# Performance work log

Hardware: AMD Instinct MI355X
Metric: run time of the kernel (lower is better)

Reference implementation:

```python
import jax, jax.numpy as jnp
import numpy as np

DIM = 192
HEADS = 6
WS = 7        # window_size
SS = 3        # shift_size
MLP_RATIO = 4.0
B = 64
H_RES = 56
W_RES = 56
EPS = 1e-5


def _rel_index(ws):
    # standard Swin relative position index, (ws*ws, ws*ws) int
    coords = np.stack(np.meshgrid(np.arange(ws), np.arange(ws), indexing='ij'))  # 2,ws,ws
    flat = coords.reshape(2, -1)                                                 # 2,N
    rel = (flat[:, :, None] - flat[:, None, :]).transpose(1, 2, 0)               # N,N,2
    rel[:, :, 0] += ws - 1
    rel[:, :, 1] += ws - 1
    rel[:, :, 0] *= 2 * ws - 1
    return rel.sum(-1)  # N,N


def _attn_mask(H, W, ws, ss):
    # (num_windows, N, N) float mask with 0 / -100, static given H,W,ws,ss
    img = np.zeros((H, W))
    sl = (slice(0, -ws), slice(-ws, -ss), slice(-ss, None))
    cnt = 0
    for hs in sl:
        for wsl in sl:
            img[hs, wsl] = cnt
            cnt += 1
    mw = img.reshape(H // ws, ws, W // ws, ws).transpose(0, 2, 1, 3).reshape(-1, ws * ws)
    diff = mw[:, None, :] - mw[:, :, None]
    return jnp.asarray(np.where(diff != 0, -100.0, 0.0).astype(np.float32))


def _ln(x, g, b):
    mu = x.mean(-1, keepdims=True)
    var = jnp.var(x, axis=-1, keepdims=True)
    return (x - mu) * jax.lax.rsqrt(var + EPS) * g + b


def setup_inputs() -> dict:
    key = jax.random.key(0)
    ks = jax.random.split(key, 8)
    C = DIM
    hid = int(C * MLP_RATIO)
    nrm = lambda k, s: jax.random.normal(k, s, jnp.float32) * 0.02
    return {
        "x": jax.random.normal(ks[0], (B, H_RES * W_RES, C), jnp.float32),
        "norm1_g": jnp.ones((C,), jnp.float32),
        "norm1_b": jnp.zeros((C,), jnp.float32),
        "qkv_w": nrm(ks[1], (3 * C, C)),
        "qkv_b": jnp.zeros((3 * C,), jnp.float32),
        "rel_bias_table": nrm(ks[2], ((2 * WS - 1) ** 2, HEADS)),
        "proj_w": nrm(ks[3], (C, C)),
        "proj_b": jnp.zeros((C,), jnp.float32),
        "norm2_g": jnp.ones((C,), jnp.float32),
        "norm2_b": jnp.zeros((C,), jnp.float32),
        "fc1_w": nrm(ks[4], (hid, C)),
        "fc1_b": jnp.zeros((hid,), jnp.float32),
        "fc2_w": nrm(ks[5], (C, hid)),
        "fc2_b": jnp.zeros((C,), jnp.float32),
        "H": H_RES,
        "W": W_RES,
    }


def _block(x, norm1_g, norm1_b, qkv_w, qkv_b, rel_bias_table, proj_w, proj_b,
           norm2_g, norm2_b, fc1_w, fc1_b, fc2_w, fc2_b, H, W):
    Bn, L, C = x.shape
    ws = min(WS, H, W)
    ss = SS if ws > SS else 0
    nH, nW = H // ws, W // ws
    N = ws * ws
    hd = C // HEADS

    shortcut = x
    h = _ln(x, norm1_g, norm1_b).reshape(Bn, H, W, C)
    if ss > 0:
        h = jnp.roll(h, (-ss, -ss), axis=(1, 2))
    # window partition -> (Bn*nH*nW, N, C)
    win = h.reshape(Bn, nH, ws, nW, ws, C).transpose(0, 1, 3, 2, 4, 5).reshape(-1, N, C)

    qkv = win @ qkv_w.T + qkv_b                       # (nWin, N, 3C)
    qkv = qkv.reshape(-1, N, 3, HEADS, hd).transpose(2, 0, 3, 1, 4)
    q, k, v = qkv[0], qkv[1], qkv[2]                  # (nWin, heads, N, hd)
    scale = float(hd) ** -0.5
    attn = jnp.einsum('whnd,whmd->whnm', q * scale, k)

    idx = _rel_index(ws)                              # N,N (static)
    bias = rel_bias_table[idx.reshape(-1)].reshape(N, N, HEADS).transpose(2, 0, 1)
    attn = attn + bias[None]

    if ss > 0:
        mask = _attn_mask(H, W, ws, ss)               # (nH*nW, N, N)
        attn = attn.reshape(Bn, nH * nW, HEADS, N, N) + mask[None, :, None]
        attn = attn.reshape(-1, HEADS, N, N)

    attn = jax.nn.softmax(attn, axis=-1)
    out = jnp.einsum('whnm,whmd->whnd', attn, v)      # (nWin, heads, N, hd)
    out = out.transpose(0, 2, 1, 3).reshape(-1, N, C)
    out = out @ proj_w.T + proj_b

    # window reverse -> (Bn, H, W, C)
    out = out.reshape(Bn, nH, nW, ws, ws, C).transpose(0, 1, 3, 2, 4, 5).reshape(Bn, H, W, C)
    if ss > 0:
        out = jnp.roll(out, (ss, ss), axis=(1, 2))
    x = shortcut + out.reshape(Bn, H * W, C)

    h2 = _ln(x, norm2_g, norm2_b)
    h2 = jax.nn.gelu(h2 @ fc1_w.T + fc1_b, approximate=False)
    h2 = h2 @ fc2_w.T + fc2_b
    return x + h2


def reference(x, norm1_g, norm1_b, qkv_w, qkv_b, rel_bias_table, proj_w, proj_b,
              norm2_g, norm2_b, fc1_w, fc1_b, fc2_w, fc2_b, H, W):
    return _block(x, norm1_g, norm1_b, qkv_w, qkv_b, rel_bias_table, proj_w, proj_b,
                  norm2_g, norm2_b, fc1_w, fc1_b, fc2_w, fc2_b, H, W)
```

## Files before the change

### kernel.cpp

```cpp
#include <hip/hip_runtime.h>
#include <hip/hip_bf16.h>
#include <math.h>

typedef __attribute__((ext_vector_type(8))) short short8;
typedef __attribute__((ext_vector_type(4))) float floatx4;

__device__ __forceinline__ float bf2f(unsigned short u) {
    union { unsigned int i; float f; } v;
    v.i = ((unsigned int)u) << 16;
    return v.f;
}
__device__ __forceinline__ unsigned short f2bf(float f) {
    union { float f; unsigned int i; } v;
    v.f = f;
    return (unsigned short)((v.i + 0x7FFFu + ((v.i >> 16) & 1u)) >> 16);
}
__device__ __forceinline__ void async16(const void* g, void* l) {
    __builtin_amdgcn_global_load_lds((const __attribute__((address_space(1))) void*)g,
                                     (__attribute__((address_space(3))) void*)l, 16, 0, 0);
}

__global__ __launch_bounds__(256) void cvt_kernel(const float* __restrict__ s,
                                                  unsigned short* __restrict__ d, int n,
                                                  int cut, float scale) {
    int i = blockIdx.x * 256 + threadIdx.x;
    if (i < n) d[i] = f2bf(s[i] * (i < cut ? scale : 1.0f));
}
__global__ __launch_bounds__(256) void biasscale_kernel(const float* __restrict__ s,
                                                        float* __restrict__ d, int n,
                                                        int cut, float scale) {
    int i = blockIdx.x * 256 + threadIdx.x;
    if (i < n) d[i] = s[i] * (i < cut ? scale : 1.0f);
}

__global__ __launch_bounds__(256) void bmt_kernel(const float* __restrict__ btab,
                                                  float* __restrict__ tbl) {
    int idx = blockIdx.x * 256 + threadIdx.x;
    int key = idx & 63;
    int q = (idx >> 6) & 63;
    int h = (idx >> 12) % 6;
    int cls = idx / (4096 * 6);
    float v;
    if (key >= 49) v = -3.0e38f;
    else if (q >= 49) v = 0.0f;
    else {
        int qi = q / 7, qj = q % 7, ki = key / 7, kj = key % 7;
        v = btab[((qi - ki + 6) * 13 + (qj - kj + 6)) * 6 + h];
        int whT = (cls >> 1) & 1, wwT = cls & 1;
        int rq = (whT ? (qi < 4 ? 1 : 2) : 0) * 3 + (wwT ? (qj < 4 ? 1 : 2) : 0);
        int rk = (whT ? (ki < 4 ? 1 : 2) : 0) * 3 + (wwT ? (kj < 4 ? 1 : 2) : 0);
        if (rq != rk) v -= 100.0f;
    }
    tbl[idx] = v;
}

__global__ __launch_bounds__(256) void ln_kernel(const float* __restrict__ src,
                                                 const float* __restrict__ gw,
                                                 const float* __restrict__ bw,
                                                 unsigned short* __restrict__ dst,
                                                 int mode) {
    int o = blockIdx.x * 4 + (threadIdx.x >> 6);
    int lane = threadIdx.x & 63;
    size_t srow;
    if (mode == 0) {
        int win = o / 49, n = o % 49;
        int b = win >> 6, wl = win & 63;
        int wh = wl >> 3, ww = wl & 7;
        int i = n / 7, j = n % 7;
        int pr = (wh * 7 + i + 3) % 56;
        int pc = (ww * 7 + j + 3) % 56;
        srow = ((size_t)b * 3136 + (size_t)(pr * 56 + pc)) * 192;
    } else {
        srow = (size_t)o * 192;
    }
    float v0 = src[srow + lane];
    float v1 = src[srow + lane + 64];
    float v2 = src[srow + lane + 128];
    float s = v0 + v1 + v2;
    float s2 = v0 * v0 + v1 * v1 + v2 * v2;
    #pragma unroll
    for (int off = 32; off > 0; off >>= 1) {
        s += __shfl_xor(s, off);
        s2 += __shfl_xor(s2, off);
    }
    float mean = s * (1.0f / 192.0f);
    float var = s2 * (1.0f / 192.0f) - mean * mean;
    float inv = rsqrtf(var + 1e-5f);
    size_t drow = (size_t)o * 192;
    dst[drow + lane]       = f2bf((v0 - mean) * inv * gw[lane]       + bw[lane]);
    dst[drow + lane + 64]  = f2bf((v1 - mean) * inv * gw[lane + 64]  + bw[lane + 64]);
    dst[drow + lane + 128] = f2bf((v2 - mean) * inv * gw[lane + 128] + bw[lane + 128]);
}

template <int EPI>
__global__ __launch_bounds__(256) void gemm_nt(const unsigned short* __restrict__ A,
                                               const unsigned short* __restrict__ W,
                                               const float* __restrict__ bias,
                                               int K, int ldo, int mbase,
                                               unsigned short* __restrict__ outb,
                                               float* __restrict__ outf,
                                               const float* __restrict__ resid) {
    __shared__ __align__(16) unsigned short Al[128][32];
    __shared__ __align__(16) unsigned short Wl[64][32];
    int tid = threadIdx.x;
    int lane = tid & 63;
    int wv = tid >> 6;
    int wm = wv >> 1, wn = wv & 1;
    int m0 = blockIdx.y * 128;
    int n0 = blockIdx.x * 64;
    int quad = lane >> 4, l15 = lane & 15;

    int srow = lane >> 2;
    int scol = (lane & 3) * 8;
    const unsigned short* aP0 = A + (size_t)(m0 + wv * 32 + srow) * K + scol;
    const unsigned short* aP1 = aP0 + (size_t)16 * K;
    const unsigned short* wP  = W + (size_t)(n0 + wv * 16 + srow) * K + scol;
    unsigned short* lA0 = &Al[wv * 32][0];
    unsigned short* lA1 = &Al[wv * 32 + 16][0];
    unsigned short* lW  = &Wl[wv * 16][0];

    floatx4 acc[4][2];
    floatx4 zero = {0.f, 0.f, 0.f, 0.f};
    #pragma unroll
    for (int a = 0; a < 4; ++a)
        #pragma unroll
        for (int b = 0; b < 2; ++b) acc[a][b] = zero;

    for (int kt = 0; kt < K; kt += 32) {
        __syncthreads();
        async16(aP0 + kt, lA0);
        async16(aP1 + kt, lA1);
        async16(wP + kt, lW);
        __syncthreads();
        short8 af[4], wf[2];
        #pragma unroll
        for (int mt = 0; mt < 4; ++mt)
            af[mt] = *(const short8*)&Al[wm * 64 + mt * 16 + l15][quad * 8];
        #pragma unroll
        for (int nt = 0; nt < 2; ++nt)
            wf[nt] = *(const short8*)&Wl[wn * 32 + nt * 16 + l15][quad * 8];
        #pragma unroll
        for (int mt = 0; mt < 4; ++mt)
            #pragma unroll
            for (int nt = 0; nt < 2; ++nt)
                acc[mt][nt] = __builtin_amdgcn_mfma_f32_16x16x32_bf16(af[mt], wf[nt], acc[mt][nt], 0, 0, 0);
    }

    #pragma unroll
    for (int mt = 0; mt < 4; ++mt) {
        #pragma unroll
        for (int nt = 0; nt < 2; ++nt) {
            #pragma unroll
            for (int r = 0; r < 4; ++r) {
                int m = m0 + wm * 64 + mt * 16 + quad * 4 + r;
                int n = n0 + wn * 32 + nt * 16 + l15;
                float v = acc[mt][nt][r] + bias[n];
                if (EPI == 0) {
                    outb[(size_t)m * ldo + n] = f2bf(v);
                } else if (EPI == 1) {
                    float g = 0.5f * v * (1.0f + erff(v * 0.70710678118654752f));
                    outb[(size_t)m * ldo + n] = f2bf(g);
                } else if (EPI == 2) {
                    int win = m / 49, np = m % 49;
                    int b = win >> 6, wl = win & 63;
                    int wh = wl >> 3, ww = wl & 7;
                    int i = np / 7, j = np % 7;
                    int pr = (wh * 7 + i + 3) % 56;
                    int pc = (ww * 7 + j + 3) % 56;
                    size_t dst = ((size_t)b * 3136 + (size_t)(pr * 56 + pc)) * 192 + n;
                    outf[dst] = resid[dst] + v;
                } else {
                    size_t dst = (size_t)(mbase + m) * ldo + n;
                    outf[dst] = resid[dst] + v;
                }
            }
        }
    }
}

__global__ __launch_bounds__(192) void attn_kernel(const unsigned short* __restrict__ qkv,
                                                   const float* __restrict__ tbl,
                                                   unsigned short* __restrict__ awin) {
    __shared__ __align__(16) unsigned short Pb[3][64][72];
    int w = blockIdx.x >> 1;
    int hb = (blockIdx.x & 1) * 3;
    int hl = threadIdx.x >> 6;
    int h = hb + hl;
    int lane = threadIdx.x & 63;
    int quad = lane >> 4, l15 = lane & 15;
    const unsigned short* base = qkv + (size_t)w * 49 * 576;
    int wl = w & 63;
    int cls = ((wl >> 3) == 7 ? 2 : 0) + ((wl & 7) == 7 ? 1 : 0);
    const float* tb = tbl + (size_t)(cls * 6 + h) * 4096;

    short8 kf[4], qf[4];
    #pragma unroll
    for (int mt = 0; mt < 4; ++mt)
        kf[mt] = *(const short8*)(base + (size_t)(mt * 16 + l15) * 576 + 192 + h * 32 + quad * 8);
    #pragma unroll
    for (int nt = 0; nt < 4; ++nt)
        qf[nt] = *(const short8*)(base + (size_t)(nt * 16 + l15) * 576 + h * 32 + quad * 8);

    floatx4 S[4][4];
    #pragma unroll
    for (int mt = 0; mt < 4; ++mt)
        #pragma unroll
        for (int nt = 0; nt < 4; ++nt) {
            floatx4 cinit = *(const floatx4*)(tb + (nt * 16 + l15) * 64 + mt * 16 + quad * 4);
            S[mt][nt] = __builtin_amdgcn_mfma_f32_16x16x32_bf16(kf[mt], qf[nt], cinit, 0, 0, 0);
        }

    #pragma unroll
    for (int mt = 0; mt < 4; ++mt)
        #pragma unroll
        for (int nt = 0; nt < 4; ++nt)
            #pragma unroll
            for (int rr = 0; rr < 4; ++rr)
                S[mt][nt][rr] = __expf(S[mt][nt][rr]);

    float rinv[4];
    #pragma unroll
    for (int nt = 0; nt < 4; ++nt) {
        float s = 0.f;
        #pragma unroll
        for (int mt = 0; mt < 4; ++mt)
            s += (S[mt][nt][0] + S[mt][nt][1]) + (S[mt][nt][2] + S[mt][nt][3]);
        s += __shfl_xor(s, 16);
        s += __shfl_xor(s, 32);
        rinv[nt] = 1.0f / s;
    }

    #pragma unroll
    for (int mt = 0; mt < 4; ++mt) {
        #pragma unroll
        for (int nt = 0; nt < 4; ++nt) {
            __hip_bfloat162 p0 = __float22bfloat162_rn(
                make_float2(S[mt][nt][0] * rinv[nt], S[mt][nt][1] * rinv[nt]));
            __hip_bfloat162 p1 = __float22bfloat162_rn(
                make_float2(S[mt][nt][2] * rinv[nt], S[mt][nt][3] * rinv[nt]));
            union { __hip_bfloat162 h2[2]; uint2 u; } pk;
            pk.h2[0] = p0;
            pk.h2[1] = p1;
            *(uint2*)&Pb[hl][nt * 16 + l15][mt * 16 + quad * 4] = pk.u;
        }
    }

    floatx4 O[4][2];
    floatx4 zero = {0.f, 0.f, 0.f, 0.f};
    #pragma unroll
    for (int mt = 0; mt < 4; ++mt)
        #pragma unroll
        for (int nt = 0; nt < 2; ++nt) O[mt][nt] = zero;
    #pragma unroll
    for (int ks = 0; ks < 2; ++ks) {
        short8 vf[2];
        #pragma unroll
        for (int nt = 0; nt < 2; ++nt) {
            const unsigned short* vb =
                base + (size_t)(ks * 32 + quad * 8) * 576 + 384 + h * 32 + nt * 16 + l15;
            #pragma unroll
            for (int j = 0; j < 8; ++j) vf[nt][j] = (short)vb[(size_t)j * 576];
        }
        #pragma unroll
        for (int mt = 0; mt < 4; ++mt) {
            short8 pf = *(const short8*)&Pb[hl][mt * 16 + l15][ks * 32 + quad * 8];
            #pragma unroll
            for (int nt = 0; nt < 2; ++nt)
                O[mt][nt] = __builtin_amdgcn_mfma_f32_16x16x32_bf16(pf, vf[nt], O[mt][nt], 0, 0, 0);
        }
    }
    #pragma unroll
    for (int mt = 0; mt < 4; ++mt) {
        #pragma unroll
        for (int rr = 0; rr < 4; ++rr) {
            int q = mt * 16 + quad * 4 + rr;
            if (q < 49) {
                #pragma unroll
                for (int nt = 0; nt < 2; ++nt)
                    awin[((size_t)w * 49 + q) * 192 + h * 32 + nt * 16 + l15] =
                        f2bf(O[mt][nt][rr]);
            }
        }
    }
}

extern "C" void kernel_launch(void* const* d_in, const int* in_sizes, int n_in,
                              void* d_out, int out_size, void* d_ws, size_t ws_size,
                              hipStream_t stream) {
    const float* x      = (const float*)d_in[0];
    const float* n1g    = (const float*)d_in[1];
    const float* n1b    = (const float*)d_in[2];
    const float* qkv_w  = (const float*)d_in[3];
    const float* qkv_b  = (const float*)d_in[4];
    const float* btab   = (const float*)d_in[5];
    const float* proj_w = (const float*)d_in[6];
    const float* proj_b = (const float*)d_in[7];
    const float* n2g    = (const float*)d_in[8];
    const float* n2b    = (const float*)d_in[9];
    const float* fc1_w  = (const float*)d_in[10];
    const float* fc1_b  = (const float*)d_in[11];
    const float* fc2_w  = (const float*)d_in[12];
    const float* fc2_b  = (const float*)d_in[13];
    float* out = (float*)d_out;

    char* p = (char*)d_ws;
    size_t off = 0;
    auto alloc = [&](size_t bytes) {
        char* r = p + off;
        off = (off + bytes + 255) & ~(size_t)255;
        return r;
    };
    unsigned short* wq   = (unsigned short*)alloc((size_t)576 * 192 * 2);
    unsigned short* wp   = (unsigned short*)alloc((size_t)192 * 192 * 2);
    unsigned short* w1   = (unsigned short*)alloc((size_t)768 * 192 * 2);
    unsigned short* w2   = (unsigned short*)alloc((size_t)192 * 768 * 2);
    unsigned short* hwin = (unsigned short*)alloc((size_t)200704 * 192 * 2);
    unsigned short* qkvb = (unsigned short*)alloc((size_t)200704 * 576 * 2);
    float*          xres = (float*)alloc((size_t)200704 * 192 * 4);
    unsigned short* g1   = (unsigned short*)alloc((size_t)50176 * 768 * 2);
    if (ws_size < off) return;
    float* tbl   = (float*)g1;
    float* qkvbs = (float*)g1 + 98304;

    const float scale = 0.17677669529663687f;
    cvt_kernel<<<432, 256, 0, stream>>>(qkv_w, wq, 110592, 36864, scale);
    cvt_kernel<<<144, 256, 0, stream>>>(proj_w, wp, 36864, 0, 1.0f);
    cvt_kernel<<<576, 256, 0, stream>>>(fc1_w, w1, 147456, 0, 1.0f);
    cvt_kernel<<<576, 256, 0, stream>>>(fc2_w, w2, 147456, 0, 1.0f);
    biasscale_kernel<<<3, 256, 0, stream>>>(qkv_b, qkvbs, 576, 192, scale);
    bmt_kernel<<<384, 256, 0, stream>>>(btab, tbl);

    ln_kernel<<<50176, 256, 0, stream>>>(x, n1g, n1b, hwin, 0);
    gemm_nt<0><<<dim3(9, 1568), 256, 0, stream>>>(hwin, wq, qkvbs, 192, 576, 0, qkvb, nullptr, nullptr);
    attn_kernel<<<8192, 192, 0, stream>>>(qkvb, tbl, hwin );
    gemm_nt<2><<<dim3(3, 1568), 256, 0, stream>>>(hwin, wp, proj_b, 192, 192, 0, nullptr, xres, x);
    unsigned short* h2 = qkvb;
    ln_kernel<<<50176, 256, 0, stream>>>(xres, n2g, n2b, h2, 1);
    for (int c = 0; c < 4; ++c) {
        int mb = c * 50176;
        gemm_nt<1><<<dim3(12, 392), 256, 0, stream>>>(h2 + (size_t)mb * 192, w1, fc1_b, 192, 768, 0,
                                                      g1, nullptr, nullptr);
        gemm_nt<3><<<dim3(3, 392), 256, 0, stream>>>(g1, w2, fc2_b, 768, 192, mb,
                                                     nullptr, out, xres);
    }
}
```

Baseline: 1.103 ms.

## Write V transposed from QKV GEMM and fuse proj GEMM with LayerNorm2

The QKV GEMM epilogue now writes V into a per-window, per-head transposed buffer, so attention loads V fragments with vector reads instead of strided scalar gathers. Q and K rows are clamped rather than read past the window. The projection GEMM is merged with the residual add and the second LayerNorm in one kernel that computes full 192-wide rows, which removes a separate LN pass over xres. h2 is written in image order and the MLP reads it from there. The cost is an extra zeroing kernel for V padding, scattered scalar V stores, and the xres buffer being reused for vT before proj_ln overwrites it.

```diff
diff --git a/kernel.cpp b/kernel.cpp
--- a/kernel.cpp
+++ b/kernel.cpp
@@ -31,6 +31,13 @@
                                                         int cut, float scale) {
     int i = blockIdx.x * 256 + threadIdx.x;
     if (i < n) d[i] = s[i] * (i < cut ? scale : 1.0f);
+}
+
+__global__ __launch_bounds__(256) void zerov_kernel(unsigned short* __restrict__ vT) {
+    int idx = blockIdx.x * 256 + threadIdx.x;
+    size_t row = (size_t)(idx >> 1);
+    uint4 z = make_uint4(0u, 0u, 0u, 0u);
+    *(uint4*)(vT + row * 64 + 48 + (idx & 1) * 8) = z;
 }
 
 __global__ __launch_bounds__(256) void bmt_kernel(const float* __restrict__ btab,
@@ -57,22 +64,16 @@
 __global__ __launch_bounds__(256) void ln_kernel(const float* __restrict__ src,
                                                  const float* __restrict__ gw,
                                                  const float* __restrict__ bw,
-                                                 unsigned short* __restrict__ dst,
-                                                 int mode) {
+                                                 unsigned short* __restrict__ dst) {
     int o = blockIdx.x * 4 + (threadIdx.x >> 6);
     int lane = threadIdx.x & 63;
-    size_t srow;
-    if (mode == 0) {
-        int win = o / 49, n = o % 49;
-        int b = win >> 6, wl = win & 63;
-        int wh = wl >> 3, ww = wl & 7;
-        int i = n / 7, j = n % 7;
-        int pr = (wh * 7 + i + 3) % 56;
-        int pc = (ww * 7 + j + 3) % 56;
-        srow = ((size_t)b * 3136 + (size_t)(pr * 56 + pc)) * 192;
-    } else {
-        srow = (size_t)o * 192;
-    }
+    int win = o / 49, n = o % 49;
+    int b = win >> 6, wl = win & 63;
+    int wh = wl >> 3, ww = wl & 7;
+    int i = n / 7, j = n % 7;
+    int pr = (wh * 7 + i + 3) % 56;
+    int pc = (ww * 7 + j + 3) % 56;
+    size_t srow = ((size_t)b * 3136 + (size_t)(pr * 56 + pc)) * 192;
     float v0 = src[srow + lane];
     float v1 = src[srow + lane + 64];
     float v2 = src[srow + lane + 128];
@@ -99,7 +100,8 @@
                                                int K, int ldo, int mbase,
                                                unsigned short* __restrict__ outb,
                                                float* __restrict__ outf,
-                                               const float* __restrict__ resid) {
+                                               const float* __restrict__ resid,
+                                               unsigned short* __restrict__ vt) {
     __shared__ __align__(16) unsigned short Al[128][32];
     __shared__ __align__(16) unsigned short Wl[64][32];
     int tid = threadIdx.x;
@@ -150,35 +152,154 @@
     for (int mt = 0; mt < 4; ++mt) {
         #pragma unroll
         for (int nt = 0; nt < 2; ++nt) {
-            #pragma unroll
-            for (int r = 0; r < 4; ++r) {
-                int m = m0 + wm * 64 + mt * 16 + quad * 4 + r;
+            if (EPI == 0 && n0 >= 384) {
                 int n = n0 + wn * 32 + nt * 16 + l15;
-                float v = acc[mt][nt][r] + bias[n];
-                if (EPI == 0) {
-                    outb[(size_t)m * ldo + n] = f2bf(v);
-                } else if (EPI == 1) {
-                    float g = 0.5f * v * (1.0f + erff(v * 0.70710678118654752f));
-                    outb[(size_t)m * ldo + n] = f2bf(g);
-                } else if (EPI == 2) {
-                    int win = m / 49, np = m % 49;
-                    int b = win >> 6, wl = win & 63;
-                    int wh = wl >> 3, ww = wl & 7;
-                    int i = np / 7, j = np % 7;
-                    int pr = (wh * 7 + i + 3) % 56;
-                    int pc = (ww * 7 + j + 3) % 56;
-                    size_t dst = ((size_t)b * 3136 + (size_t)(pr * 56 + pc)) * 192 + n;
-                    outf[dst] = resid[dst] + v;
-                } else {
-                    size_t dst = (size_t)(mbase + m) * ldo + n;
-                    outf[dst] = resid[dst] + v;
+                int nv = n - 384;
+                int hh = nv >> 5, dd = nv & 31;
+                float bv = bias[n];
+                int mq = m0 + wm * 64 + mt * 16 + quad * 4;
+                int w = mq / 49, key0 = mq - w * 49;
+                unsigned short* vrow = vt + ((size_t)(w * 6 + hh) * 32 + dd) * 64;
+                #pragma unroll
+                for (int r = 0; r < 4; ++r) {
+                    int key = key0 + r;
+                    unsigned short* dp = vrow + (key >= 49 ? key - 49 + 12288 : key);
+                    *dp = f2bf(acc[mt][nt][r] + bv);
                 }
+            } else {
+                #pragma unroll
+                for (int r = 0; r < 4; ++r) {
+                    int m = m0 + wm * 64 + mt * 16 + quad * 4 + r;
+                    int n = n0 + wn * 32 + nt * 16 + l15;
+                    float v = acc[mt][nt][r] + bias[n];
+                    if (EPI == 0) {
+                        outb[(size_t)m * ldo + n] = f2bf(v);
+                    } else if (EPI == 1) {
+                        float g = 0.5f * v * (1.0f + erff(v * 0.70710678118654752f));
+                        outb[(size_t)m * ldo + n] = f2bf(g);
+                    } else {
+                        size_t dst = (size_t)(mbase + m) * ldo + n;
+                        outf[dst] = resid[dst] + v;
+                    }
+                }
+            }
+        }
+    }
+}
+
+__global__ __launch_bounds__(256) void proj_ln_kernel(const unsigned short* __restrict__ A,
+                                                      const unsigned short* __restrict__ W,
+                                                      const float* __restrict__ bias,
+                                                      const float* __restrict__ xin,
+                                                      const float* __restrict__ g2,
+                                                      const float* __restrict__ b2,
+                                                      float* __restrict__ xres,
+                                                      unsigned short* __restrict__ h2) {
+    __shared__ __align__(16) unsigned short Al[64][32];
+    __shared__ __align__(16) unsigned short Bl[192][32];
+    __shared__ float sred[2][4][64];
+    int tid = threadIdx.x;
+    int lane = tid & 63;
+    int wv = tid >> 6;
+    int m0 = blockIdx.x * 64;
+    int quad = lane >> 4, l15 = lane & 15;
+    int srow = lane >> 2;
+    int scol = (lane & 3) * 8;
+    const unsigned short* aP = A + (size_t)(m0 + wv * 16 + srow) * 192 + scol;
+    const unsigned short* wP = W + (size_t)(wv * 48 + srow) * 192 + scol;
+
+    floatx4 acc[4][3];
+    floatx4 zero = {0.f, 0.f, 0.f, 0.f};
+    #pragma unroll
+    for (int a = 0; a < 4; ++a)
+        #pragma unroll
+        for (int b = 0; b < 3; ++b) acc[a][b] = zero;
+
+    for (int kt = 0; kt < 192; kt += 32) {
+        __syncthreads();
+        async16(aP + kt, &Al[wv * 16][0]);
+        #pragma unroll
+        for (int c = 0; c < 3; ++c)
+            async16(wP + (size_t)(c * 16) * 192 + kt, &Bl[wv * 48 + c * 16][0]);
+        __syncthreads();
+        short8 af[4], wf[3];
+        #pragma unroll
+        for (int mt = 0; mt < 4; ++mt)
+            af[mt] = *(const short8*)&Al[mt * 16 + l15][quad * 8];
+        #pragma unroll
+        for (int nt = 0; nt < 3; ++nt)
+            wf[nt] = *(const short8*)&Bl[wv * 48 + nt * 16 + l15][quad * 8];
+        #pragma unroll
+        for (int mt = 0; mt < 4; ++mt)
+            #pragma unroll
+            for (int nt = 0; nt < 3; ++nt)
+                acc[mt][nt] = __builtin_amdgcn_mfma_f32_16x16x32_bf16(af[mt], wf[nt], acc[mt][nt], 0, 0, 0);
+    }
+
+    #pragma unroll
+    for (int mt = 0; mt < 4; ++mt) {
+        #pragma unroll
+        for (int r = 0; r < 4; ++r) {
+            int m = m0 + mt * 16 + quad * 4 + r;
+            int win = m / 49, np = m % 49;
+            int b = win >> 6, wl = win & 63;
+            int wh = wl >> 3, ww = wl & 7;
+            int i = np / 7, j = np % 7;
+            int pr = (wh * 7 + i + 3) % 56;
+            int pc = (ww * 7 + j + 3) % 56;
+            size_t drow = ((size_t)b * 3136 + (size_t)(pr * 56 + pc)) * 192;
+            float ps = 0.f, pq = 0.f;
+            #pragma unroll
+            for (int nt = 0; nt < 3; ++nt) {
+                int n = wv * 48 + nt * 16 + l15;
+                float v = acc[mt][nt][r] + bias[n] + xin[drow + n];
+                acc[mt][nt][r] = v;
+                xres[drow + n] = v;
+                ps += v;
+                pq += v * v;
+            }
+            #pragma unroll
+            for (int off = 1; off < 16; off <<= 1) {
+                ps += __shfl_xor(ps, off);
+                pq += __shfl_xor(pq, off);
+            }
+            if (l15 == 0) {
+                int row = mt * 16 + quad * 4 + r;
+                sred[0][wv][row] = ps;
+                sred[1][wv][row] = pq;
+            }
+        }
+    }
+    __syncthreads();
+    #pragma unroll
+    for (int mt = 0; mt < 4; ++mt) {
+        #pragma unroll
+        for (int r = 0; r < 4; ++r) {
+            int row = mt * 16 + quad * 4 + r;
+            float s = sred[0][0][row] + sred[0][1][row] + sred[0][2][row] + sred[0][3][row];
+            float q = sred[1][0][row] + sred[1][1][row] + sred[1][2][row] + sred[1][3][row];
+            float mean = s * (1.0f / 192.0f);
+            float inv = rsqrtf(q * (1.0f / 192.0f) - mean * mean + 1e-5f);
+            int m = m0 + row;
+            int win = m / 49, np = m % 49;
+            int b = win >> 6, wl = win & 63;
+            int wh = wl >> 3, ww = wl & 7;
+            int i = np / 7, j = np % 7;
+            int pr = (wh * 7 + i + 3) % 56;
+            int pc = (ww * 7 + j + 3) % 56;
+            size_t drow = ((size_t)b * 3136 + (size_t)(pr * 56 + pc)) * 192;
+            #pragma unroll
+            for (int nt = 0; nt < 3; ++nt) {
+                int n = wv * 48 + nt * 16 + l15;
+                float v = acc[mt][nt][r];
+                h2[drow + n] = f2bf((v - mean) * inv * g2[n] + b2[n]);
             }
         }
     }
 }
 
 __global__ __launch_bounds__(192) void attn_kernel(const unsigned short* __restrict__ qkv,
+                                                   const unsigned short* __restrict__ vT,
                                                    const float* __restrict__ tbl,
                                                    unsigned short* __restrict__ awin) {
     __shared__ __align__(16) unsigned short Pb[3][64][72];
@@ -188,18 +309,32 @@
     int h = hb + hl;
     int lane = threadIdx.x & 63;
     int quad = lane >> 4, l15 = lane & 15;
-    const unsigned short* base = qkv + (size_t)w * 49 * 576;
+    const unsigned short* base = qkv + (size_t)w * 49 * 384;
     int wl = w & 63;
     int cls = ((wl >> 3) == 7 ? 2 : 0) + ((wl & 7) == 7 ? 1 : 0);
     const float* tb = tbl + (size_t)(cls * 6 + h) * 4096;
 
     short8 kf[4], qf[4];
     #pragma unroll
-    for (int mt = 0; mt < 4; ++mt)
-        kf[mt] = *(const short8*)(base + (size_t)(mt * 16 + l15) * 576 + 192 + h * 32 + quad * 8);
-    #pragma unroll
-    for (int nt = 0; nt < 4; ++nt)
-        qf[nt] = *(const short8*)(base + (size_t)(nt * 16 + l15) * 576 + h * 32 + quad * 8);
+    for (int mt = 0; mt < 4; ++mt) {
+        int krow = mt * 16 + l15;
+        krow = krow < 49 ? krow : 48;
+        kf[mt] = *(const short8*)(base + (size_t)krow * 384 + 192 + h * 32 + quad * 8);
+    }
+    #pragma unroll
+    for (int nt = 0; nt < 4; ++nt) {
+        int qrow = nt * 16 + l15;
+        qrow = qrow < 49 ? qrow : 48;
+        qf[nt] = *(const short8*)(base + (size_t)qrow * 384 + h * 32 + quad * 8);
+    }
+
+    const unsigned short* vb = vT + (size_t)(w * 6 + h) * 2048;
+    short8 vf[2][2];
+    #pragma unroll
+    for (int ks = 0; ks < 2; ++ks)
+        #pragma unroll
+        for (int nt = 0; nt < 2; ++nt)
+            vf[ks][nt] = *(const short8*)(vb + (size_t)(nt * 16 + l15) * 64 + ks * 32 + quad * 8);
 
     floatx4 S[4][4];
     #pragma unroll
@@ -253,20 +388,12 @@
         for (int nt = 0; nt < 2; ++nt) O[mt][nt] = zero;
     #pragma unroll
     for (int ks = 0; ks < 2; ++ks) {
-        short8 vf[2];
-        #pragma unroll
-        for (int nt = 0; nt < 2; ++nt) {
-            const unsigned short* vb =
-                base + (size_t)(ks * 32 + quad * 8) * 576 + 384 + h * 32 + nt * 16 + l15;
-            #pragma unroll
-            for (int j = 0; j < 8; ++j) vf[nt][j] = (short)vb[(size_t)j * 576];
-        }
         #pragma unroll
         for (int mt = 0; mt < 4; ++mt) {
             short8 pf = *(const short8*)&Pb[hl][mt * 16 + l15][ks * 32 + quad * 8];
             #pragma unroll
             for (int nt = 0; nt < 2; ++nt)
-                O[mt][nt] = __builtin_amdgcn_mfma_f32_16x16x32_bf16(pf, vf[nt], O[mt][nt], 0, 0, 0);
+                O[mt][nt] = __builtin_amdgcn_mfma_f32_16x16x32_bf16(pf, vf[ks][nt], O[mt][nt], 0, 0, 0);
         }
     }
     #pragma unroll
@@ -321,6 +448,7 @@
     if (ws_size < off) return;
     float* tbl   = (float*)g1;
     float* qkvbs = (float*)g1 + 98304;
+    unsigned short* vT = (unsigned short*)xres;
 
     const float scale = 0.17677669529663687f;
     cvt_kernel<<<432, 256, 0, stream>>>(qkv_w, wq, 110592, 36864, scale);
@@ -329,18 +457,19 @@
     cvt_kernel<<<576, 256, 0, stream>>>(fc2_w, w2, 147456, 0, 1.0f);
     biasscale_kernel<<<3, 256, 0, stream>>>(qkv_b, qkvbs, 576, 192, scale);
     bmt_kernel<<<384, 256, 0, stream>>>(btab, tbl);
-
-    ln_kernel<<<50176, 256, 0, stream>>>(x, n1g, n1b, hwin, 0);
-    gemm_nt<0><<<dim3(9, 1568), 256, 0, stream>>>(hwin, wq, qkvbs, 192, 576, 0, qkvb, nullptr, nullptr);
-    attn_kernel<<<8192, 192, 0, stream>>>(qkvb, tbl, hwin );
-    gemm_nt<2><<<dim3(3, 1568), 256, 0, stream>>>(hwin, wp, proj_b, 192, 192, 0, nullptr, xres, x);
+    zerov_kernel<<<6144, 256, 0, stream>>>(vT);
+
+    ln_kernel<<<50176, 256, 0, stream>>>(x, n1g, n1b, hwin);
+    gemm_nt<0><<<dim3(9, 1568), 256, 0, stream>>>(hwin, wq, qkvbs, 192, 384, 0,
+                                                  qkvb, nullptr, nullptr, vT);
+    attn_kernel<<<8192, 192, 0, stream>>>(qkvb, vT, tbl, hwin );
     unsigned short* h2 = qkvb;
-    ln_kernel<<<50176, 256, 0, stream>>>(xres, n2g, n2b, h2, 1);
+    proj_ln_kernel<<<3136, 256, 0, stream>>>(hwin, wp, proj_b, x, n2g, n2b, xres, h2);
     for (int c = 0; c < 4; ++c) {
         int mb = c * 50176;
         gemm_nt<1><<<dim3(12, 392), 256, 0, stream>>>(h2 + (size_t)mb * 192, w1, fc1_b, 192, 768, 0,
-                                                      g1, nullptr, nullptr);
+                                                      g1, nullptr, nullptr, nullptr);
         gemm_nt<3><<<dim3(3, 392), 256, 0, stream>>>(g1, w2, fc2_b, 768, 192, mb,
-                                                     nullptr, out, xres);
-    }
-}
+                                                     nullptr, out, xres, nullptr);
+    }
+}
```

Result: slower. 1.216 ms (+10.2%).

## Remap GEMM blocks to 1D grid with XCD-aware swizzle; clamp attention row loads

Applied to the files above, without the earlier changes.

The GEMM launches change from a 2D grid to a 1D grid. Each block's flat id is remapped so that consecutive tiles land on the same XCD (bid&7 selects the XCD chunk), which should improve L2 reuse of A rows and W tiles across MI355X's chiplets. The attention kernel also clamps Q/K row indices to 48 so the padded rows 49-63 no longer read past the window, likely avoiding out-of-bounds or redundant loads into the next window. The swizzle relies on grid sizes being divisible by 8, which all launches here are.

```diff
diff --git a/kernel.cpp b/kernel.cpp
--- a/kernel.cpp
+++ b/kernel.cpp
@@ -96,7 +96,7 @@
 __global__ __launch_bounds__(256) void gemm_nt(const unsigned short* __restrict__ A,
                                                const unsigned short* __restrict__ W,
                                                const float* __restrict__ bias,
-                                               int K, int ldo, int mbase,
+                                               int K, int ldo, int mbase, int gx,
                                                unsigned short* __restrict__ outb,
                                                float* __restrict__ outf,
                                                const float* __restrict__ resid) {
@@ -106,8 +106,10 @@
     int lane = tid & 63;
     int wv = tid >> 6;
     int wm = wv >> 1, wn = wv & 1;
-    int m0 = blockIdx.y * 128;
-    int n0 = blockIdx.x * 64;
+    int bid = blockIdx.x;
+    int v = (bid & 7) * ((int)gridDim.x >> 3) + (bid >> 3);
+    int m0 = (v / gx) * 128;
+    int n0 = (v % gx) * 64;
     int quad = lane >> 4, l15 = lane & 15;
 
     int srow = lane >> 2;
@@ -154,11 +156,11 @@
             for (int r = 0; r < 4; ++r) {
                 int m = m0 + wm * 64 + mt * 16 + quad * 4 + r;
                 int n = n0 + wn * 32 + nt * 16 + l15;
-                float v = acc[mt][nt][r] + bias[n];
+                float v2 = acc[mt][nt][r] + bias[n];
                 if (EPI == 0) {
-                    outb[(size_t)m * ldo + n] = f2bf(v);
+                    outb[(size_t)m * ldo + n] = f2bf(v2);
                 } else if (EPI == 1) {
-                    float g = 0.5f * v * (1.0f + erff(v * 0.70710678118654752f));
+                    float g = 0.5f * v2 * (1.0f + erff(v2 * 0.70710678118654752f));
                     outb[(size_t)m * ldo + n] = f2bf(g);
                 } else if (EPI == 2) {
                     int win = m / 49, np = m % 49;
@@ -168,10 +170,10 @@
                     int pr = (wh * 7 + i + 3) % 56;
                     int pc = (ww * 7 + j + 3) % 56;
                     size_t dst = ((size_t)b * 3136 + (size_t)(pr * 56 + pc)) * 192 + n;
-                    outf[dst] = resid[dst] + v;
+                    outf[dst] = resid[dst] + v2;
                 } else {
                     size_t dst = (size_t)(mbase + m) * ldo + n;
-                    outf[dst] = resid[dst] + v;
+                    outf[dst] = resid[dst] + v2;
                 }
             }
         }
@@ -195,11 +197,17 @@
 
     short8 kf[4], qf[4];
     #pragma unroll
-    for (int mt = 0; mt < 4; ++mt)
-        kf[mt] = *(const short8*)(base + (size_t)(mt * 16 + l15) * 576 + 192 + h * 32 + quad * 8);
-    #pragma unroll
-    for (int nt = 0; nt < 4; ++nt)
-        qf[nt] = *(const short8*)(base + (size_t)(nt * 16 + l15) * 576 + h * 32 + quad * 8);
+    for (int mt = 0; mt < 4; ++mt) {
+        int krow = mt * 16 + l15;
+        krow = krow < 49 ? krow : 48;
+        kf[mt] = *(const short8*)(base + (size_t)krow * 576 + 192 + h * 32 + quad * 8);
+    }
+    #pragma unroll
+    for (int nt = 0; nt < 4; ++nt) {
+        int qrow = nt * 16 + l15;
+        qrow = qrow < 49 ? qrow : 48;
+        qf[nt] = *(const short8*)(base + (size_t)qrow * 576 + h * 32 + quad * 8);
+    }
 
     floatx4 S[4][4];
     #pragma unroll
@@ -331,16 +339,18 @@
     bmt_kernel<<<384, 256, 0, stream>>>(btab, tbl);
 
     ln_kernel<<<50176, 256, 0, stream>>>(x, n1g, n1b, hwin, 0);
-    gemm_nt<0><<<dim3(9, 1568), 256, 0, stream>>>(hwin, wq, qkvbs, 192, 576, 0, qkvb, nullptr, nullptr);
+    gemm_nt<0><<<14112, 256, 0, stream>>>(hwin, wq, qkvbs, 192, 576, 0, 9,
+                                          qkvb, nullptr, nullptr);
     attn_kernel<<<8192, 192, 0, stream>>>(qkvb, tbl, hwin );
-    gemm_nt<2><<<dim3(3, 1568), 256, 0, stream>>>(hwin, wp, proj_b, 192, 192, 0, nullptr, xres, x);
+    gemm_nt<2><<<4704, 256, 0, stream>>>(hwin, wp, proj_b, 192, 192, 0, 3,
+                                         nullptr, xres, x);
     unsigned short* h2 = qkvb;
     ln_kernel<<<50176, 256, 0, stream>>>(xres, n2g, n2b, h2, 1);
     for (int c = 0; c < 4; ++c) {
         int mb = c * 50176;
-        gemm_nt<1><<<dim3(12, 392), 256, 0, stream>>>(h2 + (size_t)mb * 192, w1, fc1_b, 192, 768, 0,
-                                                      g1, nullptr, nullptr);
-        gemm_nt<3><<<dim3(3, 392), 256, 0, stream>>>(g1, w2, fc2_b, 768, 192, mb,
-                                                     nullptr, out, xres);
-    }
-}
+        gemm_nt<1><<<4704, 256, 0, stream>>>(h2 + (size_t)mb * 192, w1, fc1_b, 192, 768, 0, 12,
+                                             g1, nullptr, nullptr);
+        gemm_nt<3><<<1176, 256, 0, stream>>>(g1, w2, fc2_b, 768, 192, mb, 3,
+                                             nullptr, out, xres);
+    }
+}
```

Result: faster. 1.039 ms (-5.8%).
